# Optimization experiments

Hardware: AMD Instinct MI355X
Metric: run time of the kernel (lower is better)

Reference implementation:

```python
import jax, jax.numpy as jnp
import numpy as np

D_MODEL = 1024
D_STATE = 128
D_CONV = 4
EXPAND = 2
HEADDIM = 64
D_INNER = EXPAND * D_MODEL          # 2048
NHEADS = D_INNER // HEADDIM          # 32
CONV_CH = D_INNER + 2 * D_STATE      # conv acts on x, B, C (ngroups=1)
D_IN_PROJ = 2 * D_INNER + 2 * D_STATE + NHEADS
CHUNK = 128


def setup_inputs() -> dict:
    key = jax.random.key(0)
    ks = jax.random.split(key, 8)
    B, L = 4, 2048
    return {
        'x': jax.random.normal(ks[0], (B, L, D_MODEL), jnp.float32),
        'ln_w': jnp.ones((D_MODEL,), jnp.float32),
        'ln_b': jnp.zeros((D_MODEL,), jnp.float32),
        'in_proj_w': jax.random.normal(ks[1], (D_IN_PROJ, D_MODEL), jnp.float32) * 0.02,
        'conv_w': jax.random.normal(ks[2], (CONV_CH, D_CONV), jnp.float32) * 0.2,
        'conv_b': jnp.zeros((CONV_CH,), jnp.float32),
        'dt_bias': jax.random.normal(ks[3], (NHEADS,), jnp.float32) * 0.5,
        'A_log': jax.random.uniform(ks[4], (NHEADS,), jnp.float32, 0.0, 1.5),
        'D': jax.random.normal(ks[5], (NHEADS,), jnp.float32) * 0.1 + 1.0,
        'norm_w': jnp.ones((D_INNER,), jnp.float32),
        'out_proj_w': jax.random.normal(ks[6], (D_MODEL, D_INNER), jnp.float32) * 0.02,
    }


def segsum(a):
    # a: (..., T) -> (..., T, T) with out[i, j] = sum_{j < k <= i} a[k], -inf above diag
    T = a.shape[-1]
    a_rep = jnp.broadcast_to(a[..., :, None], a.shape + (T,))
    a_masked = jnp.where(jnp.tril(jnp.ones((T, T), bool), -1), a_rep, 0.0)
    seg = jnp.cumsum(a_masked, axis=-2)
    return jnp.where(jnp.tril(jnp.ones((T, T), bool), 0), seg, -jnp.inf)


def _ssd(X, a, Bm, Cm):
    # Chunked SSD (Mamba2). X: (b,l,h,p) pre-multiplied by dt; a: (b,l,h)=dt*A; Bm,Cm: (b,l,n)
    b, l, h, p = X.shape
    c = l // CHUNK
    Xc = X.reshape(b, c, CHUNK, h, p)
    Bc = Bm.reshape(b, c, CHUNK, -1)
    Cc = Cm.reshape(b, c, CHUNK, -1)
    ac = a.reshape(b, c, CHUNK, h).transpose(0, 3, 1, 2)   # (b,h,c,q)
    a_cs = jnp.cumsum(ac, axis=-1)                          # (b,h,c,q)
    Lm = jnp.exp(segsum(ac))                                # (b,h,c,q,q)
    # intra-chunk (diagonal) part
    Y_diag = jnp.einsum('bcln,bcsn,bhcls,bcshp->bclhp', Cc, Bc, Lm, Xc)
    # chunk final states
    decay_states = jnp.exp(a_cs[..., -1:] - a_cs)           # (b,h,c,q)
    states = jnp.einsum('bcln,bhcl,bclhp->bchpn', Bc, decay_states, Xc)
    states = jnp.concatenate([jnp.zeros_like(states[:, :1]), states], axis=1)  # (b,c+1,h,p,n)
    a_chunk = jnp.pad(a_cs[..., -1], ((0, 0), (0, 0), (1, 0)))  # (b,h,c+1)
    decay_chunk = jnp.exp(segsum(a_chunk))                  # (b,h,c+1,c+1)
    prev_states = jnp.einsum('bhzc,bchpn->bzhpn', decay_chunk, states)[:, :-1]  # (b,c,h,p,n)
    # inter-chunk (off-diagonal) part
    Y_off = jnp.einsum('bcln,bchpn,bhcl->bclhp', Cc, prev_states, jnp.exp(a_cs))
    return (Y_diag + Y_off).reshape(b, l, h, p)


def reference(x, ln_w, ln_b, in_proj_w, conv_w, conv_b, dt_bias, A_log, D, norm_w, out_proj_w):
    B, L, _ = x.shape
    # pre-LayerNorm
    mu = x.mean(-1, keepdims=True)
    var = ((x - mu) ** 2).mean(-1, keepdims=True)
    h = (x - mu) / jnp.sqrt(var + 1e-5) * ln_w + ln_b
    # Mamba2 in_proj -> [z, xBC, dt]
    zxbcdt = h @ in_proj_w.T
    z = zxbcdt[..., :D_INNER]
    xBC = zxbcdt[..., D_INNER:D_INNER + CONV_CH]
    dt = jax.nn.softplus(zxbcdt[..., -NHEADS:] + dt_bias)  # (B,L,H)
    # causal depthwise conv1d + SiLU
    xp = jnp.pad(xBC, ((0, 0), (D_CONV - 1, 0), (0, 0)))
    conv = sum(xp[:, k:k + L, :] * conv_w[:, k] for k in range(D_CONV)) + conv_b
    xBC = jax.nn.silu(conv)
    xs = xBC[..., :D_INNER].reshape(B, L, NHEADS, HEADDIM)
    Bm = xBC[..., D_INNER:D_INNER + D_STATE]
    Cm = xBC[..., D_INNER + D_STATE:]
    A = -jnp.exp(A_log)                                    # (H,)
    Y = _ssd(xs * dt[..., None], dt * A, Bm, Cm)
    Y = Y + D[None, None, :, None] * xs                    # D skip connection
    y = Y.reshape(B, L, D_INNER)
    # gated RMSNorm (norm_before_gate=False)
    y = y * jax.nn.silu(z)
    y = y * jax.lax.rsqrt(jnp.mean(y * y, -1, keepdims=True) + 1e-5) * norm_w
    out = y @ out_proj_w.T
    # dropout in eval mode = identity; residual
    return out + x
```

## Files before the change

kernel.cpp:

```cpp
#include <hip/hip_runtime.h>
#include <math.h>

#define BATCH   4
#define LSEQ    2048
#define DMODEL  1024
#define DSTATE  128
#define HEADDIM 64
#define DINNER  2048
#define NHEADS  32
#define CONVCH  2304
#define DINPROJ 4384
#define NPAD    4480
#define CHUNKL  128
#define NCHUNK  16
#define ROWS    (BATCH*LSEQ)

#define B_Z     ((size_t)0)
#define B_XBC   (B_Z   + (size_t)ROWS*DINNER*2)
#define B_DT    (B_XBC + (size_t)ROWS*CONVCH*2)
#define B_XS    (B_DT  + (size_t)ROWS*NHEADS*4)
#define B_BC    (B_XS  + (size_t)ROWS*DINNER*2)
#define B_Y     (B_BC  + (size_t)ROWS*256*2)
#define B_ASUM  (B_Y   + (size_t)ROWS*DINNER*2)
#define B_END   (B_ASUM + (size_t)BATCH*NCHUNK*NHEADS*4)

typedef __attribute__((ext_vector_type(8))) short bf16x8;
typedef __attribute__((ext_vector_type(4))) float f32x4;

__device__ __forceinline__ float b2f(ushort u) {
  union { uint32_t i; float f; } v; v.i = ((uint32_t)u) << 16; return v.f;
}
__device__ __forceinline__ ushort f2b(float f) {
  union { float f; uint32_t i; } v; v.f = f;
  uint32_t r = (v.i + 0x7FFFu + ((v.i >> 16) & 1u)) >> 16;
  return (ushort)r;
}

__device__ __forceinline__ void async_ld16(const void* g, void* l) {
  __builtin_amdgcn_global_load_lds(
      (const __attribute__((address_space(1))) unsigned int*)g,
      (__attribute__((address_space(3))) unsigned int*)l, 16, 0, 0);
}

template<int K>
__device__ __forceinline__ void gemm_core_swz(const ushort* __restrict__ A,
    const ushort* __restrict__ W, int m0, int n0, int tid,
    ushort* lA, ushort* lB, f32x4 acc[4][4])
{
  const int lane = tid & 63;
  const int w = tid >> 6;
  const int wm = (w & 1) * 64;
  const int wn = (w >> 1) * 64;
  const int rl = lane & 15;
  const int q  = lane >> 4;
  for (int k0 = 0; k0 < K; k0 += 64) {
    __syncthreads();
    #pragma unroll
    for (int is = 0; is < 4; is++) {
      int s = (w*4 + is)*64 + lane;
      int row = s >> 3;
      int g = (s & 7) ^ (row & 7);
      async_ld16(A + (size_t)(m0 + row)*K + k0 + g*8, lA + (size_t)s*8);
      async_ld16(W + (size_t)(n0 + row)*K + k0 + g*8, lB + (size_t)s*8);
    }
    __syncthreads();
    #pragma unroll
    for (int kh = 0; kh < 2; kh++) {
      bf16x8 af[4], bfr[4];
      #pragma unroll
      for (int i = 0; i < 4; i++) {
        int row = wm + i*16 + rl;
        af[i] = *(const bf16x8*)&lA[(size_t)(row*8 + ((kh*4 + q) ^ (row & 7)))*8];
      }
      #pragma unroll
      for (int j = 0; j < 4; j++) {
        int row = wn + j*16 + rl;
        bfr[j] = *(const bf16x8*)&lB[(size_t)(row*8 + ((kh*4 + q) ^ (row & 7)))*8];
      }
      #pragma unroll
      for (int i = 0; i < 4; i++)
        #pragma unroll
        for (int j = 0; j < 4; j++)
          acc[i][j] = __builtin_amdgcn_mfma_f32_16x16x32_bf16(af[i], bfr[j], acc[i][j], 0, 0, 0);
    }
  }
}

__global__ __launch_bounds__(256) void convert_win_kernel(const float* __restrict__ W,
                                                          ushort* __restrict__ Wb)
{
  size_t i = (size_t)blockIdx.x*256 + threadIdx.x;
  Wb[i] = (i < (size_t)DINPROJ*DMODEL) ? f2b(W[i]) : (ushort)0;
}

__global__ __launch_bounds__(256) void convert_wout_kernel(const float* __restrict__ W,
                                                           ushort* __restrict__ Wb)
{
  size_t i = (size_t)blockIdx.x*256 + threadIdx.x;
  Wb[i] = f2b(W[i]);
}

__global__ __launch_bounds__(256) void ln_kernel(const float* __restrict__ x,
    const float* __restrict__ w, const float* __restrict__ bias, ushort* __restrict__ h)
{
  const int row = blockIdx.x;
  const int t = threadIdx.x;
  const float* xr = x + (size_t)row * DMODEL;
  float v[4];
  float s = 0.f;
  #pragma unroll
  for (int i = 0; i < 4; i++) { v[i] = xr[t + i*256]; s += v[i]; }
  __shared__ float red[4];
  #pragma unroll
  for (int o = 32; o > 0; o >>= 1) s += __shfl_down(s, o, 64);
  if ((t & 63) == 0) red[t >> 6] = s;
  __syncthreads();
  float mean = (red[0]+red[1]+red[2]+red[3]) * (1.f/DMODEL);
  float vs = 0.f;
  #pragma unroll
  for (int i = 0; i < 4; i++) { float d = v[i]-mean; vs += d*d; }
  #pragma unroll
  for (int o = 32; o > 0; o >>= 1) vs += __shfl_down(vs, o, 64);
  __syncthreads();
  if ((t & 63) == 0) red[t >> 6] = vs;
  __syncthreads();
  float rstd = rsqrtf((red[0]+red[1]+red[2]+red[3]) * (1.f/DMODEL) + 1e-5f);
  ushort* hr = h + (size_t)row * DMODEL;
  #pragma unroll
  for (int i = 0; i < 4; i++) {
    int c = t + i*256;
    hr[c] = f2b((v[i]-mean)*rstd*w[c] + bias[c]);
  }
}

__global__ __launch_bounds__(256) void gemm_inproj_mfma(const ushort* __restrict__ A,
    const ushort* __restrict__ W, ushort* __restrict__ z, ushort* __restrict__ xbc,
    float* __restrict__ dtr, const float* __restrict__ dtb)
{
  __shared__ ushort smem[16384];
  ushort* lA = smem;
  ushort* lB = smem + 8192;
  const int tid = threadIdx.x;
  const int lane = tid & 63;
  const int w = tid >> 6;
  const int m0 = blockIdx.x * 128;
  const int n0 = blockIdx.y * 128;
  const int wm = (w & 1) * 64;
  const int wn = (w >> 1) * 64;
  f32x4 acc[4][4];
  #pragma unroll
  for (int i = 0; i < 4; i++)
    #pragma unroll
    for (int j = 0; j < 4; j++) acc[i][j] = (f32x4)(0.f);

  gemm_core_swz<DMODEL>(A, W, m0, n0, tid, lA, lB, acc);

  const int col_l = lane & 15;
  const int row_l = (lane >> 4) * 4;
  __syncthreads();
  if (n0 < DINNER + CONVCH) {
    #pragma unroll
    for (int i = 0; i < 4; i++)
      #pragma unroll
      for (int j = 0; j < 4; j++) {
        int col = wn + j*16 + col_l;
        int g = col >> 3;
        #pragma unroll
        for (int r = 0; r < 4; r++) {
          int row = wm + i*16 + row_l + r;
          smem[row*128 + ((g ^ (row & 7)) << 3) + (col & 7)] = f2b(acc[i][j][r]);
        }
      }
    __syncthreads();
    ushort* outp; int coff, ncols;
    if (n0 < DINNER) { outp = z;   coff = n0;          ncols = DINNER; }
    else             { outp = xbc; coff = n0 - DINNER; ncols = CONVCH; }
    #pragma unroll
    for (int it = 0; it < 8; it++) {
      int idx = tid + it*256;
      int row = idx >> 4, c8 = idx & 15;
      *(uint4*)(outp + (size_t)(m0 + row)*ncols + coff + c8*8) =
          *(const uint4*)&smem[row*128 + ((c8 ^ (row & 7)) << 3)];
    }
  } else {
    #pragma unroll
    for (int i = 0; i < 4; i++)
      #pragma unroll
      for (int j = 0; j < 2; j++) {
        int lc = wn + j*16 + col_l;
        if (lc < 32) {
          float bb = dtb[lc];
          #pragma unroll
          for (int r = 0; r < 4; r++) {
            float v = acc[i][j][r] + bb;
            v = (v > 20.f) ? v : log1pf(expf(v));
            dtr[(size_t)(m0 + wm + i*16 + row_l + r)*NHEADS + lc] = v;
          }
        }
      }
  }
}

__global__ __launch_bounds__(256) void gemm_outproj_mfma(const ushort* __restrict__ A,
    const ushort* __restrict__ W, const float* __restrict__ x, float* __restrict__ out)
{
  __shared__ ushort smem[16384];
  ushort* lA = smem;
  ushort* lB = smem + 8192;
  float* fbuf = (float*)smem;
  const int tid = threadIdx.x;
  const int lane = tid & 63;
  const int w = tid >> 6;
  const int m0 = blockIdx.x * 128;
  const int n0 = blockIdx.y * 128;
  const int wn = (w >> 1) * 64;
  f32x4 acc[4][4];
  #pragma unroll
  for (int i = 0; i < 4; i++)
    #pragma unroll
    for (int j = 0; j < 4; j++) acc[i][j] = (f32x4)(0.f);

  gemm_core_swz<DINNER>(A, W, m0, n0, tid, lA, lB, acc);

  const int colL = lane & 15;
  const int rowQ = (lane >> 4) * 4;
  #pragma unroll
  for (int h0 = 0; h0 < 2; h0++) {
    __syncthreads();
    if ((w & 1) == h0) {
      #pragma unroll
      for (int i = 0; i < 4; i++)
        #pragma unroll
        for (int j = 0; j < 4; j++) {
          int col = wn + j*16 + colL;
          int g = col >> 2;
          #pragma unroll
          for (int r = 0; r < 4; r++) {
            int row = i*16 + rowQ + r;
            fbuf[row*128 + ((g ^ (row & 7)) << 2) + (col & 3)] = acc[i][j][r];
          }
        }
    }
    __syncthreads();
    #pragma unroll
    for (int it = 0; it < 8; it++) {
      int idx = tid + it*256;
      int row = idx >> 5, c4 = idx & 31;
      int gm = m0 + h0*64 + row;
      float4 xv = *(const float4*)(x + (size_t)gm*DMODEL + n0 + c4*4);
      float4 vv = *(const float4*)&fbuf[row*128 + ((c4 ^ (row & 7)) << 2)];
      vv.x += xv.x; vv.y += xv.y; vv.z += xv.z; vv.w += xv.w;
      *(float4*)(out + (size_t)gm*DMODEL + n0 + c4*4) = vv;
    }
  }
}

__global__ __launch_bounds__(256) void conv_tiled(const ushort* __restrict__ xbc,
    const float* __restrict__ cw, const float* __restrict__ cb,
    ushort* __restrict__ xs, ushort* __restrict__ bcb)
{
  __shared__ ushort tile[35*256];
  const int tid = threadIdx.x;
  const int ch0 = blockIdx.x * 256;
  const int row0 = blockIdx.y * 32;
  const int l0 = row0 & (LSEQ-1);
  for (int idx = tid; idx < 35*32; idx += 256) {
    int r = idx >> 5, c16 = idx & 31;
    uint4 v = make_uint4(0,0,0,0);
    if (l0 + r - 3 >= 0)
      v = *(const uint4*)(xbc + (size_t)(row0 + r - 3)*CONVCH + ch0 + c16*8);
    *(uint4*)&tile[r*256 + c16*8] = v;
  }
  __syncthreads();
  const int ch = ch0 + tid;
  const float w0 = cw[ch*4+0], w1 = cw[ch*4+1], w2 = cw[ch*4+2], w3 = cw[ch*4+3];
  const float bias = cb[ch];
  const bool isX = (ch0 < DINNER);
  #pragma unroll 4
  for (int r = 0; r < 32; r++) {
    float acc = bias;
    acc = fmaf(b2f(tile[(r+0)*256 + tid]), w0, acc);
    acc = fmaf(b2f(tile[(r+1)*256 + tid]), w1, acc);
    acc = fmaf(b2f(tile[(r+2)*256 + tid]), w2, acc);
    acc = fmaf(b2f(tile[(r+3)*256 + tid]), w3, acc);
    float v = acc / (1.f + expf(-acc));
    if (isX) xs[(size_t)(row0 + r)*DINNER + ch] = f2b(v);
    else     bcb[(size_t)(row0 + r)*256 + (ch - DINNER)] = f2b(v);
  }
}

__global__ __launch_bounds__(256) void states_mfma(
    const ushort* __restrict__ xs, const ushort* __restrict__ bcb, const float* __restrict__ dt,
    const float* __restrict__ A_log, ushort* __restrict__ S, float* __restrict__ asum)
{
  constexpr int LDP = 136;
  __shared__ ushort lBT[128*LDP];
  __shared__ ushort lXT[64*LDP];
  __shared__ float dts[CHUNKL], acs[CHUNKL];
  __shared__ float wtot;
  const int hh = blockIdx.x, c = blockIdx.y, b = blockIdx.z;
  const int tid = threadIdx.x;
  const int lane = tid & 63;
  const int w = tid >> 6;
  const int rbase = b*LSEQ + c*CHUNKL;
  const size_t sbase = (size_t)((b*NCHUNK + c)*NHEADS + hh) * 8192;

  float pre = 0.f;
  if (tid < 128) {
    float myv = dt[(size_t)(rbase + tid)*NHEADS + hh];
    dts[tid] = myv;
    pre = myv;
    #pragma unroll
    for (int o = 1; o < 64; o <<= 1) {
      float u = __shfl_up(pre, o, 64);
      if ((tid & 63) >= o) pre += u;
    }
    if (tid == 63) wtot = pre;
  }
  #pragma unroll
  for (int it = 0; it < 8; it++) {
    int chunk = tid + it*256;
    int l = chunk >> 4, n8 = chunk & 15;
    ushort tmp[8];
    *(uint4*)tmp = *(const uint4*)(bcb + (size_t)(rbase + l)*256 + n8*8);
    #pragma unroll
    for (int u = 0; u < 8; u++) lBT[(n8*8+u)*LDP + l] = tmp[u];
  }
  __syncthreads();
  float alast_loc = 0.f;
  if (tid < 128) {
    float Aval = -expf(A_log[hh]);
    float a = (pre + ((tid >= 64) ? wtot : 0.f)) * Aval;
    acs[tid] = a;
    if (tid == 127) { asum[(b*NCHUNK + c)*NHEADS + hh] = a; }
  }
  __syncthreads();
  alast_loc = acs[CHUNKL-1];
  #pragma unroll
  for (int it = 0; it < 4; it++) {
    int chunk = tid + it*256;
    int l = chunk >> 3, p8 = (chunk & 7)*8;
    ushort tmp[8];
    *(uint4*)tmp = *(const uint4*)(xs + (size_t)(rbase + l)*DINNER + hh*HEADDIM + p8);
    float wl = dts[l] * expf(alast_loc - acs[l]);
    #pragma unroll
    for (int u = 0; u < 8; u++) lXT[(p8+u)*LDP + l] = f2b(b2f(tmp[u]) * wl);
  }
  __syncthreads();

  const int rl = lane & 15;
  const int kq = (lane >> 4) * 8;
  const int nb = w * 32;
  f32x4 acc[4][2];
  #pragma unroll
  for (int i = 0; i < 4; i++) { acc[i][0] = (f32x4)(0.f); acc[i][1] = (f32x4)(0.f); }
  #pragma unroll
  for (int k0 = 0; k0 < 128; k0 += 32) {
    bf16x8 af[4], bfr[2];
    #pragma unroll
    for (int i = 0; i < 4; i++) af[i]  = *(const bf16x8*)&lXT[(i*16 + rl)*LDP + k0 + kq];
    #pragma unroll
    for (int j = 0; j < 2; j++) bfr[j] = *(const bf16x8*)&lBT[(nb + j*16 + rl)*LDP + k0 + kq];
    #pragma unroll
    for (int i = 0; i < 4; i++)
      #pragma unroll
      for (int j = 0; j < 2; j++)
        acc[i][j] = __builtin_amdgcn_mfma_f32_16x16x32_bf16(af[i], bfr[j], acc[i][j], 0, 0, 0);
  }
  __syncthreads();
  const int colL = lane & 15;
  const int rowQ = (lane >> 4) * 4;
  #pragma unroll
  for (int i = 0; i < 4; i++)
    #pragma unroll
    for (int j = 0; j < 2; j++)
      #pragma unroll
      for (int r = 0; r < 4; r++)
        lXT[(i*16 + rowQ + r)*LDP + nb + j*16 + colL] = f2b(acc[i][j][r]);
  __syncthreads();
  #pragma unroll
  for (int it = 0; it < 4; it++) {
    int idx = tid + it*256;
    int row = idx >> 4, c8 = idx & 15;
    *(uint4*)(S + sbase + row*128 + c8*8) = *(const uint4*)&lXT[row*LDP + c8*8];
  }
}

__global__ __launch_bounds__(256) void scan_kernel(ushort* __restrict__ S, const float* __restrict__ asum)
{
  const int hh = blockIdx.x, sl = blockIdx.y, b = blockIdx.z;
  const int base0 = sl*2048 + threadIdx.x;
  float carry[8];
  #pragma unroll
  for (int i = 0; i < 8; i++) carry[i] = 0.f;
  for (int c = 0; c < NCHUNK; c++) {
    ushort* Sp = S + (size_t)((b*NCHUNK + c)*NHEADS + hh) * 8192;
    float dec = expf(asum[(b*NCHUNK + c)*NHEADS + hh]);
    #pragma unroll
    for (int i = 0; i < 8; i++) {
      int idx = base0 + i*256;
      float sv = b2f(Sp[idx]);
      Sp[idx] = f2b(carry[i]);
      carry[i] = fmaf(dec, carry[i], sv);
    }
  }
}

__global__ __launch_bounds__(256) void yssd_mfma(
    const ushort* __restrict__ xs, const ushort* __restrict__ bcb, const float* __restrict__ dt,
    const float* __restrict__ A_log, const float* __restrict__ Dvec,
    const ushort* __restrict__ S, ushort* __restrict__ y)
{
  constexpr int LDP = 136;
  __shared__ ushort lM [128*LDP];
  __shared__ ushort lXT[64*LDP];
  __shared__ float dts[CHUNKL], acs[CHUNKL];
  __shared__ float wtot;
  const int hh = blockIdx.x, c = blockIdx.y, b = blockIdx.z;
  const int tid = threadIdx.x;
  const int lane = tid & 63;
  const int w = tid >> 6;
  const int rbase = b*LSEQ + c*CHUNKL;
  const size_t sbase = (size_t)((b*NCHUNK + c)*NHEADS + hh) * 8192;
  const ushort* Bg = bcb + (size_t)rbase*256;
  const ushort* Cg = Bg + 128;

  #pragma unroll
  for (int it = 0; it < 4; it++) {
    int chunk = tid + it*256;
    int s = chunk >> 3, p0 = (chunk & 7)*8;
    ushort tmp[8];
    *(uint4*)tmp = *(const uint4*)(xs + (size_t)(rbase + s)*DINNER + hh*HEADDIM + p0);
    #pragma unroll
    for (int u = 0; u < 8; u++) lXT[(p0+u)*LDP + s] = tmp[u];
  }
  float pre = 0.f;
  if (tid < 128) {
    float myv = dt[(size_t)(rbase + tid)*NHEADS + hh];
    dts[tid] = myv;
    pre = myv;
    #pragma unroll
    for (int o = 1; o < 64; o <<= 1) {
      float u = __shfl_up(pre, o, 64);
      if ((tid & 63) >= o) pre += u;
    }
    if (tid == 63) wtot = pre;
  }
  __syncthreads();
  if (tid < 128) {
    float Aval = -expf(A_log[hh]);
    acs[tid] = (pre + ((tid >= 64) ? wtot : 0.f)) * Aval;
  }

  const int rl = lane & 15;
  const int kq = (lane >> 4) * 8;
  const int colL = lane & 15;
  const int rowQ = (lane >> 4) * 4;

  const int wm = (w & 1) * 64;
  const int wn = (w >> 1) * 64;
  f32x4 G[4][4];
  #pragma unroll
  for (int i = 0; i < 4; i++)
    #pragma unroll
    for (int j = 0; j < 4; j++) G[i][j] = (f32x4)(0.f);
  #pragma unroll
  for (int k0 = 0; k0 < 128; k0 += 32) {
    bf16x8 af[4], bfr[4];
    #pragma unroll
    for (int i = 0; i < 4; i++) af[i]  = *(const bf16x8*)(Cg + (size_t)(wm + i*16 + rl)*256 + k0 + kq);
    #pragma unroll
    for (int j = 0; j < 4; j++) bfr[j] = *(const bf16x8*)(Bg + (size_t)(wn + j*16 + rl)*256 + k0 + kq);
    #pragma unroll
    for (int i = 0; i < 4; i++)
      #pragma unroll
      for (int j = 0; j < 4; j++)
        G[i][j] = __builtin_amdgcn_mfma_f32_16x16x32_bf16(af[i], bfr[j], G[i][j], 0, 0, 0);
  }
  __syncthreads();

  #pragma unroll
  for (int j = 0; j < 4; j++) {
    int sIdx = wn + j*16 + colL;
    float as = acs[sIdx];
    float ds = dts[sIdx];
    #pragma unroll
    for (int i = 0; i < 4; i++) {
      #pragma unroll
      for (int r = 0; r < 4; r++) {
        int lIdx = wm + i*16 + rowQ + r;
        float m = (lIdx >= sIdx) ? G[i][j][r] * expf(acs[lIdx] - as) * ds : 0.f;
        lM[lIdx*LDP + sIdx] = f2b(m);
      }
    }
  }

  const int om = w * 32;
  f32x4 Y[2][4];
  #pragma unroll
  for (int i = 0; i < 2; i++)
    #pragma unroll
    for (int j = 0; j < 4; j++) Y[i][j] = (f32x4)(0.f);
  #pragma unroll
  for (int k0 = 0; k0 < 128; k0 += 32) {
    bf16x8 a2[2], b2[4];
    #pragma unroll
    for (int i = 0; i < 2; i++) a2[i] = *(const bf16x8*)(Cg + (size_t)(om + i*16 + rl)*256 + k0 + kq);
    #pragma unroll
    for (int j = 0; j < 4; j++) b2[j] = *(const bf16x8*)(S + sbase + (size_t)(j*16 + rl)*128 + k0 + kq);
    #pragma unroll
    for (int i = 0; i < 2; i++)
      #pragma unroll
      for (int j = 0; j < 4; j++)
        Y[i][j] = __builtin_amdgcn_mfma_f32_16x16x32_bf16(a2[i], b2[j], Y[i][j], 0, 0, 0);
  }
  #pragma unroll
  for (int i = 0; i < 2; i++)
    #pragma unroll
    for (int r = 0; r < 4; r++) {
      float e = expf(acs[om + i*16 + rowQ + r]);
      #pragma unroll
      for (int j = 0; j < 4; j++) Y[i][j][r] *= e;
    }
  __syncthreads();

  #pragma unroll
  for (int k0 = 0; k0 < 128; k0 += 32) {
    bf16x8 a3[2], b3[4];
    #pragma unroll
    for (int i = 0; i < 2; i++) a3[i] = *(const bf16x8*)&lM[(om + i*16 + rl)*LDP + k0 + kq];
    #pragma unroll
    for (int j = 0; j < 4; j++) b3[j] = *(const bf16x8*)&lXT[(j*16 + rl)*LDP + k0 + kq];
    #pragma unroll
    for (int i = 0; i < 2; i++)
      #pragma unroll
      for (int j = 0; j < 4; j++)
        Y[i][j] = __builtin_amdgcn_mfma_f32_16x16x32_bf16(a3[i], b3[j], Y[i][j], 0, 0, 0);
  }

  const float Dh = Dvec[hh];
  #pragma unroll
  for (int i = 0; i < 2; i++) {
    #pragma unroll
    for (int r = 0; r < 4; r++) {
      int lIdx = om + i*16 + rowQ + r;
      ushort* yrow = y + (size_t)(rbase + lIdx)*DINNER + hh*HEADDIM;
      #pragma unroll
      for (int j = 0; j < 4; j++) {
        int p = j*16 + colL;
        float val = Y[i][j][r] + Dh * b2f(lXT[p*LDP + lIdx]);
        yrow[p] = f2b(val);
      }
    }
  }
}

__global__ __launch_bounds__(256) void rmsnorm_kernel(ushort* __restrict__ y,
    const ushort* __restrict__ z, const float* __restrict__ nw)
{
  const int row = blockIdx.x;
  const int t = threadIdx.x;
  ushort* yr = y + (size_t)row*DINNER;
  const ushort* zr = z + (size_t)row*DINNER;
  float v[8];
  float ss = 0.f;
  #pragma unroll
  for (int i = 0; i < 8; i++) {
    int c = t + i*256;
    float zz = b2f(zr[c]);
    float g = b2f(yr[c]) * (zz / (1.f + expf(-zz)));
    v[i] = g;
    ss += g*g;
  }
  #pragma unroll
  for (int o = 32; o > 0; o >>= 1) ss += __shfl_down(ss, o, 64);
  __shared__ float red[4];
  if ((t & 63) == 0) red[t >> 6] = ss;
  __syncthreads();
  float scale = rsqrtf((red[0]+red[1]+red[2]+red[3]) * (1.f/DINNER) + 1e-5f);
  #pragma unroll
  for (int i = 0; i < 8; i++) {
    int c = t + i*256;
    yr[c] = f2b(v[i]*scale*nw[c]);
  }
}

extern "C" void kernel_launch(void* const* d_in, const int* in_sizes, int n_in,
                              void* d_out, int out_size, void* d_ws, size_t ws_size,
                              hipStream_t stream)
{
  const float* x    = (const float*)d_in[0];
  const float* lnw  = (const float*)d_in[1];
  const float* lnb  = (const float*)d_in[2];
  const float* win  = (const float*)d_in[3];
  const float* cw   = (const float*)d_in[4];
  const float* cb   = (const float*)d_in[5];
  const float* dtb  = (const float*)d_in[6];
  const float* alog = (const float*)d_in[7];
  const float* dvec = (const float*)d_in[8];
  const float* nw   = (const float*)d_in[9];
  const float* wout = (const float*)d_in[10];
  float* out = (float*)d_out;
  char* ws = (char*)d_ws;
  (void)in_sizes; (void)n_in; (void)out_size;

  if (ws_size < B_END) return;

  ushort* zb   = (ushort*)(ws + B_Z);
  ushort* xbcb = (ushort*)(ws + B_XBC);
  float*  dtr  = (float*) (ws + B_DT);
  ushort* xsb  = (ushort*)(ws + B_XS);
  ushort* bcb  = (ushort*)(ws + B_BC);
  ushort* yb   = (ushort*)(ws + B_Y);
  float*  asum = (float*) (ws + B_ASUM);
  ushort* Sb   = xbcb;
  ushort* hb   = yb;
  ushort* winB = (ushort*)(ws + B_Y + (size_t)ROWS*DMODEL*2);
  ushort* woutB= (ushort*)(ws + B_XBC + (size_t)BATCH*NCHUNK*NHEADS*HEADDIM*DSTATE*2);

  hipLaunchKernelGGL(convert_win_kernel, dim3((NPAD*DMODEL)/256), dim3(256), 0, stream, win, winB);
  hipLaunchKernelGGL(ln_kernel, dim3(ROWS), dim3(256), 0, stream, x, lnw, lnb, hb);
  hipLaunchKernelGGL(gemm_inproj_mfma, dim3(64, 35), dim3(256), 0, stream, hb, winB, zb, xbcb, dtr, dtb);
  hipLaunchKernelGGL(conv_tiled, dim3(9, ROWS/32), dim3(256), 0, stream, xbcb, cw, cb, xsb, bcb);
  hipLaunchKernelGGL(convert_wout_kernel, dim3((DMODEL*DINNER)/256), dim3(256), 0, stream, wout, woutB);
  hipLaunchKernelGGL(states_mfma, dim3(NHEADS, NCHUNK, BATCH), dim3(256), 0, stream,
                     xsb, bcb, dtr, alog, Sb, asum);
  hipLaunchKernelGGL(scan_kernel, dim3(NHEADS, 4, BATCH), dim3(256), 0, stream, Sb, asum);
  hipLaunchKernelGGL(yssd_mfma, dim3(NHEADS, NCHUNK, BATCH), dim3(256), 0, stream,
                     xsb, bcb, dtr, alog, dvec, Sb, yb);
  hipLaunchKernelGGL(rmsnorm_kernel, dim3(ROWS), dim3(256), 0, stream, yb, zb, nw);
  hipLaunchKernelGGL(gemm_outproj_mfma, dim3(64, 8), dim3(256), 0, stream, yb, woutB, x, out);
}
```

Baseline: 493.6 us.

## Use 256x128 double-buffered 512-thread GEMMs with XCD-aware block remapping

Both projection GEMMs move from 128x128 tiles with 256 threads to 256x128 tiles with 512 threads. The K-loop is double-buffered in LDS, so the async global-to-LDS load of the next tile overlaps the MFMA work on the current one, with s_setprio raised around the compute. Block indices are remapped so neighbouring tiles land on the same XCD for better L2 reuse. This removes the load/compute serialization and the extra barrier of the old single-buffered loop, at the cost of 96KB LDS per block and a larger tile that may reduce occupancy.

```diff
diff --git a/kernel.cpp b/kernel.cpp
--- a/kernel.cpp
+++ b/kernel.cpp
@@ -42,47 +42,50 @@
       (__attribute__((address_space(3))) unsigned int*)l, 16, 0, 0);
 }
 
+
 template<int K>
-__device__ __forceinline__ void gemm_core_swz(const ushort* __restrict__ A,
-    const ushort* __restrict__ W, int m0, int n0, int tid,
-    ushort* lA, ushort* lB, f32x4 acc[4][4])
-{
-  const int lane = tid & 63;
-  const int w = tid >> 6;
-  const int wm = (w & 1) * 64;
-  const int wn = (w >> 1) * 64;
-  const int rl = lane & 15;
-  const int q  = lane >> 4;
-  for (int k0 = 0; k0 < K; k0 += 64) {
-    __syncthreads();
-    #pragma unroll
-    for (int is = 0; is < 4; is++) {
-      int s = (w*4 + is)*64 + lane;
-      int row = s >> 3;
-      int g = (s & 7) ^ (row & 7);
-      async_ld16(A + (size_t)(m0 + row)*K + k0 + g*8, lA + (size_t)s*8);
-      async_ld16(W + (size_t)(n0 + row)*K + k0 + g*8, lB + (size_t)s*8);
-    }
-    __syncthreads();
-    #pragma unroll
-    for (int kh = 0; kh < 2; kh++) {
-      bf16x8 af[4], bfr[4];
-      #pragma unroll
-      for (int i = 0; i < 4; i++) {
-        int row = wm + i*16 + rl;
-        af[i] = *(const bf16x8*)&lA[(size_t)(row*8 + ((kh*4 + q) ^ (row & 7)))*8];
-      }
-      #pragma unroll
-      for (int j = 0; j < 4; j++) {
-        int row = wn + j*16 + rl;
-        bfr[j] = *(const bf16x8*)&lB[(size_t)(row*8 + ((kh*4 + q) ^ (row & 7)))*8];
-      }
-      #pragma unroll
-      for (int i = 0; i < 4; i++)
-        #pragma unroll
-        for (int j = 0; j < 4; j++)
-          acc[i][j] = __builtin_amdgcn_mfma_f32_16x16x32_bf16(af[i], bfr[j], acc[i][j], 0, 0, 0);
-    }
+__device__ __forceinline__ void stage_tile(const ushort* __restrict__ A,
+    const ushort* __restrict__ W, int m0, int n0, int tid, int t,
+    ushort* lA, ushort* lB)
+{
+  const int k0 = t * 64;
+  #pragma unroll
+  for (int it = 0; it < 4; it++) {
+    int s = it*512 + tid;
+    int row = s >> 3;
+    int g = (s & 7) ^ (row & 7);
+    async_ld16(A + (size_t)(m0 + row)*K + k0 + g*8, lA + (size_t)s*8);
+  }
+  #pragma unroll
+  for (int it = 0; it < 2; it++) {
+    int s = it*512 + tid;
+    int row = s >> 3;
+    int g = (s & 7) ^ (row & 7);
+    async_ld16(W + (size_t)(n0 + row)*K + k0 + g*8, lB + (size_t)s*8);
+  }
+}
+
+__device__ __forceinline__ void compute_tile(const ushort* lA, const ushort* lB,
+    int wr, int wc, int rl, int q, f32x4 acc[4][4])
+{
+  #pragma unroll
+  for (int kh = 0; kh < 2; kh++) {
+    bf16x8 af[4], bfr[4];
+    #pragma unroll
+    for (int i = 0; i < 4; i++) {
+      int row = wr*64 + i*16 + rl;
+      af[i] = *(const bf16x8*)&lA[(size_t)(row*8 + ((kh*4 + q) ^ (row & 7)))*8];
+    }
+    #pragma unroll
+    for (int j = 0; j < 4; j++) {
+      int row = wc*64 + j*16 + rl;
+      bfr[j] = *(const bf16x8*)&lB[(size_t)(row*8 + ((kh*4 + q) ^ (row & 7)))*8];
+    }
+    #pragma unroll
+    for (int i = 0; i < 4; i++)
+      #pragma unroll
+      for (int j = 0; j < 4; j++)
+        acc[i][j] = __builtin_amdgcn_mfma_f32_16x16x32_bf16(af[i], bfr[j], acc[i][j], 0, 0, 0);
   }
 }
 
@@ -133,41 +136,60 @@
   }
 }
 
-__global__ __launch_bounds__(256) void gemm_inproj_mfma(const ushort* __restrict__ A,
+__global__ __launch_bounds__(512, 2) void gemm_inproj_big(const ushort* __restrict__ A,
     const ushort* __restrict__ W, ushort* __restrict__ z, ushort* __restrict__ xbc,
     float* __restrict__ dtr, const float* __restrict__ dtb)
 {
-  __shared__ ushort smem[16384];
-  ushort* lA = smem;
-  ushort* lB = smem + 8192;
+  __shared__ ushort smem[49152];
+  ushort* lA0 = smem;
+  ushort* lB0 = smem + 32768;
   const int tid = threadIdx.x;
   const int lane = tid & 63;
   const int w = tid >> 6;
-  const int m0 = blockIdx.x * 128;
-  const int n0 = blockIdx.y * 128;
-  const int wm = (w & 1) * 64;
-  const int wn = (w >> 1) * 64;
+  const int wr = w >> 1;
+  const int wc = w & 1;
+  const int rl = lane & 15;
+  const int q  = lane >> 4;
+
+  int orig = blockIdx.y*32 + blockIdx.x;
+  int wgid = (orig & 7)*140 + (orig >> 3);
+  const int m0 = (wgid & 31) * 256;
+  const int n0 = (wgid >> 5) * 128;
+
   f32x4 acc[4][4];
   #pragma unroll
   for (int i = 0; i < 4; i++)
     #pragma unroll
     for (int j = 0; j < 4; j++) acc[i][j] = (f32x4)(0.f);
 
-  gemm_core_swz<DMODEL>(A, W, m0, n0, tid, lA, lB, acc);
-
-  const int col_l = lane & 15;
-  const int row_l = (lane >> 4) * 4;
-  __syncthreads();
+  constexpr int NT = DMODEL / 64;
+  stage_tile<DMODEL>(A, W, m0, n0, tid, 0, lA0, lB0);
+  __syncthreads();
+  for (int t = 0; t < NT; t++) {
+    ushort* cA = lA0 + (size_t)(t & 1) * 16384;
+    ushort* cB = lB0 + (size_t)(t & 1) * 8192;
+    if (t + 1 < NT)
+      stage_tile<DMODEL>(A, W, m0, n0, tid, t + 1,
+                         lA0 + (size_t)((t+1) & 1) * 16384,
+                         lB0 + (size_t)((t+1) & 1) * 8192);
+    __builtin_amdgcn_s_setprio(1);
+    compute_tile(cA, cB, wr, wc, rl, q, acc);
+    __builtin_amdgcn_s_setprio(0);
+    __syncthreads();
+  }
+
+  const int colL = lane & 15;
+  const int rowQ = (lane >> 4) * 4;
   if (n0 < DINNER + CONVCH) {
     #pragma unroll
     for (int i = 0; i < 4; i++)
       #pragma unroll
       for (int j = 0; j < 4; j++) {
-        int col = wn + j*16 + col_l;
+        int col = wc*64 + j*16 + colL;
         int g = col >> 3;
         #pragma unroll
         for (int r = 0; r < 4; r++) {
-          int row = wm + i*16 + row_l + r;
+          int row = wr*64 + i*16 + rowQ + r;
           smem[row*128 + ((g ^ (row & 7)) << 3) + (col & 7)] = f2b(acc[i][j][r]);
         }
       }
@@ -177,66 +199,87 @@
     else             { outp = xbc; coff = n0 - DINNER; ncols = CONVCH; }
     #pragma unroll
     for (int it = 0; it < 8; it++) {
-      int idx = tid + it*256;
+      int idx = tid + it*512;
       int row = idx >> 4, c8 = idx & 15;
       *(uint4*)(outp + (size_t)(m0 + row)*ncols + coff + c8*8) =
           *(const uint4*)&smem[row*128 + ((c8 ^ (row & 7)) << 3)];
     }
   } else {
-    #pragma unroll
-    for (int i = 0; i < 4; i++)
-      #pragma unroll
-      for (int j = 0; j < 2; j++) {
-        int lc = wn + j*16 + col_l;
-        if (lc < 32) {
+    if (wc == 0) {
+      #pragma unroll
+      for (int i = 0; i < 4; i++)
+        #pragma unroll
+        for (int j = 0; j < 2; j++) {
+          int lc = j*16 + colL;
           float bb = dtb[lc];
           #pragma unroll
           for (int r = 0; r < 4; r++) {
             float v = acc[i][j][r] + bb;
             v = (v > 20.f) ? v : log1pf(expf(v));
-            dtr[(size_t)(m0 + wm + i*16 + row_l + r)*NHEADS + lc] = v;
+            dtr[(size_t)(m0 + wr*64 + i*16 + rowQ + r)*NHEADS + lc] = v;
           }
         }
-      }
-  }
-}
-
-__global__ __launch_bounds__(256) void gemm_outproj_mfma(const ushort* __restrict__ A,
+    }
+  }
+}
+
+__global__ __launch_bounds__(512, 2) void gemm_outproj_big(const ushort* __restrict__ A,
     const ushort* __restrict__ W, const float* __restrict__ x, float* __restrict__ out)
 {
-  __shared__ ushort smem[16384];
-  ushort* lA = smem;
-  ushort* lB = smem + 8192;
+  __shared__ ushort smem[49152];
+  ushort* lA0 = smem;
+  ushort* lB0 = smem + 32768;
   float* fbuf = (float*)smem;
   const int tid = threadIdx.x;
   const int lane = tid & 63;
   const int w = tid >> 6;
-  const int m0 = blockIdx.x * 128;
-  const int n0 = blockIdx.y * 128;
-  const int wn = (w >> 1) * 64;
+  const int wr = w >> 1;
+  const int wc = w & 1;
+  const int rl = lane & 15;
+  const int q  = lane >> 4;
+
+  int orig = blockIdx.y*32 + blockIdx.x;
+  int wgid = (orig & 7)*32 + (orig >> 3);
+  const int m0 = (wgid & 31) * 256;
+  const int n0 = (wgid >> 5) * 128;
+
   f32x4 acc[4][4];
   #pragma unroll
   for (int i = 0; i < 4; i++)
     #pragma unroll
     for (int j = 0; j < 4; j++) acc[i][j] = (f32x4)(0.f);
 
-  gemm_core_swz<DINNER>(A, W, m0, n0, tid, lA, lB, acc);
+  constexpr int NT = DINNER / 64;
+  stage_tile<DINNER>(A, W, m0, n0, tid, 0, lA0, lB0);
+  __syncthreads();
+  for (int t = 0; t < NT; t++) {
+    ushort* cA = lA0 + (size_t)(t & 1) * 16384;
+    ushort* cB = lB0 + (size_t)(t & 1) * 8192;
+    if (t + 1 < NT)
+      stage_tile<DINNER>(A, W, m0, n0, tid, t + 1,
+                         lA0 + (size_t)((t+1) & 1) * 16384,
+                         lB0 + (size_t)((t+1) & 1) * 8192);
+    __builtin_amdgcn_s_setprio(1);
+    compute_tile(cA, cB, wr, wc, rl, q, acc);
+    __builtin_amdgcn_s_setprio(0);
+    __syncthreads();
+  }
 
   const int colL = lane & 15;
   const int rowQ = (lane >> 4) * 4;
   #pragma unroll
-  for (int h0 = 0; h0 < 2; h0++) {
+  for (int h = 0; h < 2; h++) {
     __syncthreads();
-    if ((w & 1) == h0) {
+    if ((wr >> 1) == h) {
       #pragma unroll
       for (int i = 0; i < 4; i++)
         #pragma unroll
         for (int j = 0; j < 4; j++) {
-          int col = wn + j*16 + colL;
+          int col = wc*64 + j*16 + colL;
           int g = col >> 2;
           #pragma unroll
           for (int r = 0; r < 4; r++) {
-            int row = i*16 + rowQ + r;
+            int row = (wr & 1)*64 + i*16 + rowQ + r;
             fbuf[row*128 + ((g ^ (row & 7)) << 2) + (col & 3)] = acc[i][j][r];
           }
         }
@@ -244,9 +287,9 @@
     __syncthreads();
     #pragma unroll
     for (int it = 0; it < 8; it++) {
-      int idx = tid + it*256;
+      int idx = tid + it*512;
       int row = idx >> 5, c4 = idx & 31;
-      int gm = m0 + h0*64 + row;
+      int gm = m0 + h*128 + row;
       float4 xv = *(const float4*)(x + (size_t)gm*DMODEL + n0 + c4*4);
       float4 vv = *(const float4*)&fbuf[row*128 + ((c4 ^ (row & 7)) << 2)];
       vv.x += xv.x; vv.y += xv.y; vv.z += xv.z; vv.w += xv.w;
@@ -620,7 +663,7 @@
 
   hipLaunchKernelGGL(convert_win_kernel, dim3((NPAD*DMODEL)/256), dim3(256), 0, stream, win, winB);
   hipLaunchKernelGGL(ln_kernel, dim3(ROWS), dim3(256), 0, stream, x, lnw, lnb, hb);
-  hipLaunchKernelGGL(gemm_inproj_mfma, dim3(64, 35), dim3(256), 0, stream, hb, winB, zb, xbcb, dtr, dtb);
+  hipLaunchKernelGGL(gemm_inproj_big, dim3(32, 35), dim3(512), 0, stream, hb, winB, zb, xbcb, dtr, dtb);
   hipLaunchKernelGGL(conv_tiled, dim3(9, ROWS/32), dim3(256), 0, stream, xbcb, cw, cb, xsb, bcb);
   hipLaunchKernelGGL(convert_wout_kernel, dim3((DMODEL*DINNER)/256), dim3(256), 0, stream, wout, woutB);
   hipLaunchKernelGGL(states_mfma, dim3(NHEADS, NCHUNK, BATCH), dim3(256), 0, stream,
@@ -629,5 +672,5 @@
   hipLaunchKernelGGL(yssd_mfma, dim3(NHEADS, NCHUNK, BATCH), dim3(256), 0, stream,
                      xsb, bcb, dtr, alog, dvec, Sb, yb);
   hipLaunchKernelGGL(rmsnorm_kernel, dim3(ROWS), dim3(256), 0, stream, yb, zb, nw);
-  hipLaunchKernelGGL(gemm_outproj_mfma, dim3(64, 8), dim3(256), 0, stream, yb, woutB, x, out);
-}
+  hipLaunchKernelGGL(gemm_outproj_big, dim3(32, 8), dim3(512), 0, stream, yb, woutB, x, out);
+}
```

After: 474.7 us. 1.04x faster.
